# Optimization experiments

Measured on AMD Instinct MI355X. Metric: run time of the kernel, lower is better.

The kernel has to match this reference:

```python
import jax, jax.numpy as jnp
import numpy as np

DIM = 192
HEADS = 8
EPS = 1e-12  # torch F.normalize eps


def setup_inputs() -> dict:
    key = jax.random.key(0)
    k1, k2, k3, k4 = jax.random.split(key, 4)
    b, c, h, w = 2, DIM, 256, 256
    x = jax.random.normal(k1, (b, c, h, w), dtype=jnp.float32)
    # 1x1 conv weights stored as (out, in)
    qkv_w = jax.random.normal(k2, (3 * c, c), dtype=jnp.float32) * (1.0 / np.sqrt(c))
    # depthwise 3x3, groups = 3c -> OIHW with I=1
    dw_w = jax.random.normal(k3, (3 * c, 1, 3, 3), dtype=jnp.float32) * (1.0 / 3.0)
    proj_w = jax.random.normal(k4, (c, c), dtype=jnp.float32) * (1.0 / np.sqrt(c))
    temperature = jnp.ones((HEADS, 1, 1), dtype=jnp.float32)
    return {"x": x, "qkv_w": qkv_w, "dw_w": dw_w, "proj_w": proj_w,
            "temperature": temperature}


def _l2norm(t):
    n = jnp.sqrt(jnp.sum(t * t, axis=-1, keepdims=True))
    return t / jnp.maximum(n, EPS)


def reference(x, qkv_w, dw_w, proj_w, temperature):
    b, c, h, w = x.shape
    # 1x1 conv (pointwise) -> depthwise 3x3 conv
    qkv = jnp.einsum('oc,bchw->bohw', qkv_w, x)  # (b, 3c, h, w)
    qkv = jax.lax.conv_general_dilated(
        qkv, dw_w, window_strides=(1, 1), padding='SAME',
        feature_group_count=3 * c,
        dimension_numbers=('NCHW', 'OIHW', 'NCHW'))
    q, k, v = jnp.split(qkv, 3, axis=1)
    # faithful reshape: full C channels per head, spatial dim split by heads
    q = q.reshape(b, HEADS, c, -1)
    k = k.reshape(b, HEADS, c, -1)
    v = v.reshape(b, HEADS, c, -1)
    q = _l2norm(q)
    k = _l2norm(k)
    attn = jnp.einsum('bhcn,bhdn->bhcd', q, k) * temperature  # (b,H,c,c)
    attn = jax.nn.softmax(attn, axis=-1)
    out = jnp.einsum('bhcd,bhdn->bhcn', attn, v)
    out = out.reshape(b, c, h, w)
    out = jnp.einsum('oc,bchw->bohw', proj_w, out)
    return out
```

## Files before the change

### kernel.cpp

```cpp
#include <hip/hip_runtime.h>
#include <math.h>

typedef unsigned short u16;
typedef unsigned int   u32;
typedef short bf16x8 __attribute__((ext_vector_type(8)));
typedef float f32x4  __attribute__((ext_vector_type(4)));
typedef u16 u16x8 __attribute__((ext_vector_type(8)));
typedef u32 u32x4 __attribute__((ext_vector_type(4)));

#define MFMA16(a,b,c) __builtin_amdgcn_mfma_f32_16x16x32_bf16((a),(b),(c),0,0,0)

__device__ __forceinline__ float bf2f(u16 h){ u32 u=((u32)h)<<16; return __uint_as_float(u); }
__device__ __forceinline__ u16 f2bf(float f){ u32 u=__float_as_uint(f); return (u16)((u+0x7fffu+((u>>16)&1u))>>16); }
__device__ __forceinline__ u32 pack2(float a, float b){ return (u32)f2bf(a) | ((u32)f2bf(b)<<16); }

__device__ __forceinline__ void gl2lds(const u16* g, u16* l){
  __builtin_amdgcn_global_load_lds((const __attribute__((address_space(1))) u32*)g,
                                   (__attribute__((address_space(3))) u32*)l, 16, 0, 0);
}
__device__ __forceinline__ void stc(u16* p, float v){ *p = f2bf(v); }
__device__ __forceinline__ void stc(float* p, float v){ *p = v; }
__device__ __forceinline__ void ld4(const u16* p, float* v){ ushort4 x=*(const ushort4*)p; v[0]=bf2f(x.x);v[1]=bf2f(x.y);v[2]=bf2f(x.z);v[3]=bf2f(x.w); }

__device__ __forceinline__ int xcd_remap(){
  int gx = gridDim.x, gy = gridDim.y;
  int lin = blockIdx.x + gx*(blockIdx.y + gy*blockIdx.z);
  int nwg = gx*gy*gridDim.z;
  if (nwg & 7) return lin;
  int q = nwg >> 3;
  return (lin & 7)*q + (lin >> 3);
}

__global__ void prep_kernel(const float* __restrict__ qkv_w, const float* __restrict__ proj_w,
                            u16* __restrict__ wq, u16* __restrict__ wp, float* __restrict__ norms){
  int i = blockIdx.x*256 + threadIdx.x;
  if (i < 110592) wq[i] = f2bf(qkv_w[i]);
  else if (i < 147456) wp[i-110592] = f2bf(proj_w[i-110592]);
  else if (i < 156672) norms[i-147456] = 0.f;
}

__global__ __launch_bounds__(256) void transpose_kernel(
    const u16* __restrict__ in, u16* __restrict__ out,
    long in_hi, long in_lo, long out_slab, int in_pitch)
{
  __shared__ float tile[64][65];
  const int t = threadIdx.x;
  const int z = blockIdx.z;
  const u16* ip = in + (long)(z>>3)*in_hi + (long)(z&7)*in_lo;
  u16* op = out + (long)z*out_slab;
  const int s0 = blockIdx.x*64, c0 = blockIdx.y*64;
  const int rl = t>>4, cc = (t&15)*4;
#pragma unroll
  for (int rr=0; rr<4; rr++){
    int row = rr*16 + rl;
    float v[4];
    ld4(ip + (long)(c0+row)*in_pitch + s0 + cc, v);
    tile[row][cc+0]=v[0]; tile[row][cc+1]=v[1]; tile[row][cc+2]=v[2]; tile[row][cc+3]=v[3];
  }
  __syncthreads();
#pragma unroll
  for (int wr=0; wr<4; wr++){
    int sl = wr*16 + rl;
    ushort4 s;
    s.x = f2bf(tile[cc+0][sl]); s.y = f2bf(tile[cc+1][sl]);
    s.z = f2bf(tile[cc+2][sl]); s.w = f2bf(tile[cc+3][sl]);
    *(ushort4*)(op + (long)(s0+sl)*192 + c0 + cc) = s;
  }
}

__global__ __launch_bounds__(256) void gemm_qkv_kernel(
    const u16* __restrict__ A, const float* __restrict__ X, u16* __restrict__ C)
{
  __shared__ __align__(16) u16 As[128*32];
  __shared__ __align__(16) u16 Bs[128*36];
  const int t = threadIdx.x, w = t>>6, l = t&63;
  const int wrk = xcd_remap();
  const int mt = wrk % 5;
  const int rest = wrk / 5;
  const int nt = rest % 512, bz = rest / 512;
  const int m0 = mt*128, n0 = nt*128;
  const float* Xb = X + (long)bz*12582912L + n0;
  const int rq = t>>2, qq = (t&3)*8;
  int ar0 = m0 + rq;      if (ar0 >= 576) ar0 = 575;
  int ar1 = m0 + 64 + rq; if (ar1 >= 576) ar1 = 575;
  const int bq = t&31;
  const int kb = (t>>5)*4;
  f32x4 acc[4][4];
#pragma unroll
  for (int i=0;i<4;i++)
#pragma unroll
    for (int j=0;j<4;j++) acc[i][j] = f32x4{0.f,0.f,0.f,0.f};

  for (int k0=0; k0<192; k0+=32){
    __syncthreads();
    float xv[4][4];
#pragma unroll
    for (int i=0;i<4;i++){
      const float* xr = Xb + (long)(k0+kb+i)*65536 + bq;
#pragma unroll
      for (int c=0;c<4;c++) xv[i][c] = xr[c*32];
    }
    gl2lds(A + (long)ar0*192 + k0 + qq, As + t*8);
    gl2lds(A + (long)ar1*192 + k0 + qq, As + (256+t)*8);
#pragma unroll
    for (int c=0;c<4;c++){
      u16* bw = Bs + (bq + c*32)*36 + kb;
      *(u32*)(bw)     = pack2(xv[0][c], xv[1][c]);
      *(u32*)(bw + 2) = pack2(xv[2][c], xv[3][c]);
    }
    __syncthreads();
    const u16* ap = As + ((w>>1)*64 + (l&15))*32 + (l>>4)*8;
    const u16* bp = Bs + ((w&1)*64 + (l&15))*36 + (l>>4)*8;
    bf16x8 a[4], b[4];
#pragma unroll
    for (int i=0;i<4;i++) a[i] = *(const bf16x8*)(ap + i*512);
#pragma unroll
    for (int j=0;j<4;j++){
      uint2 p0 = *(const uint2*)(bp + j*576);
      uint2 p1 = *(const uint2*)(bp + j*576 + 4);
      u32x4 tv = {p0.x, p0.y, p1.x, p1.y};
      b[j] = __builtin_bit_cast(bf16x8, tv);
    }
#pragma unroll
    for (int i=0;i<4;i++)
#pragma unroll
      for (int j=0;j<4;j++) acc[i][j] = MFMA16(a[i], b[j], acc[i][j]);
  }
  const int mw = m0 + (w>>1)*64, nw = n0 + (w&1)*64;
  u16* Cb = C + (long)bz*37748736L;
#pragma unroll
  for (int i=0;i<4;i++){
#pragma unroll
    for (int r=0;r<4;r++){
      int row = mw + i*16 + (l>>4)*4 + r;
      if (row < 576){
        u16* cp = Cb + (long)row*65536 + nw + (l&15);
#pragma unroll
        for (int j=0;j<4;j++) stc(cp + j*16, acc[i][j][r]);
      }
    }
  }
}

template<typename TC>
__global__ __launch_bounds__(256) void gemm_nt_kernel(
    const u16* __restrict__ A, const u16* __restrict__ B, TC* __restrict__ C,
    int M, long sB, long sC)
{
  __shared__ __align__(16) u16 As[128*32];
  __shared__ __align__(16) u16 Bs[128*32];
  const int t = threadIdx.x, w = t>>6, l = t&63;
  const int wrk = xcd_remap();
  const int mt = wrk % gridDim.x;
  const int rest = wrk / gridDim.x;
  const int nt = rest % gridDim.y, bz = rest / gridDim.y;
  const int m0 = mt*128, n0 = nt*128;
  const u16* Bb = B + (long)bz*sB + (long)n0*192;
  const int rq = t>>2, qq = (t&3)*8;
  int ar0 = m0 + rq;      if (ar0 >= M) ar0 = M-1;
  int ar1 = m0 + 64 + rq; if (ar1 >= M) ar1 = M-1;
  f32x4 acc[4][4];
#pragma unroll
  for (int i=0;i<4;i++)
#pragma unroll
    for (int j=0;j<4;j++) acc[i][j] = f32x4{0.f,0.f,0.f,0.f};

  for (int k0=0; k0<192; k0+=32){
    __syncthreads();
    gl2lds(A + (long)ar0*192 + k0 + qq, As + t*8);
    gl2lds(A + (long)ar1*192 + k0 + qq, As + (256+t)*8);
    gl2lds(Bb + (long)rq*192 + k0 + qq, Bs + t*8);
    gl2lds(Bb + (long)(64+rq)*192 + k0 + qq, Bs + (256+t)*8);
    __syncthreads();
    const u16* ap = As + ((w>>1)*64 + (l&15))*32 + (l>>4)*8;
    const u16* bp = Bs + ((w&1)*64 + (l&15))*32 + (l>>4)*8;
    bf16x8 a[4], b[4];
#pragma unroll
    for (int i=0;i<4;i++){ a[i] = *(const bf16x8*)(ap + i*512); b[i] = *(const bf16x8*)(bp + i*512); }
#pragma unroll
    for (int i=0;i<4;i++)
#pragma unroll
      for (int j=0;j<4;j++) acc[i][j] = MFMA16(a[i], b[j], acc[i][j]);
  }
  const int mw = m0 + (w>>1)*64, nw = n0 + (w&1)*64;
  TC* Cb = C + (long)bz*sC;
#pragma unroll
  for (int i=0;i<4;i++){
#pragma unroll
    for (int r=0;r<4;r++){
      int row = mw + i*16 + (l>>4)*4 + r;
      if (row < M){
        TC* cp = Cb + (long)row*65536 + nw + (l&15);
#pragma unroll
        for (int j=0;j<4;j++) stc(cp + j*16, acc[i][j][r]);
      }
    }
  }
}

__global__ __launch_bounds__(256) void dwconv_kernel(
    const u16* __restrict__ in, const float* __restrict__ w9s,
    u16* __restrict__ out, float* __restrict__ norms)
{
  const int bo = blockIdx.x >> 1;
  const int half = blockIdx.x & 1;
  const int o  = bo % 576;
  const int t = threadIdx.x, wv = t>>6, l = t&63;
  const int q = l&31;
  const int r0 = half*128 + wv*32 + (l>>5)*16;
  const u16* ip = in + (long)bo*65536L + q*8;
  u16* op = out + (long)bo*65536L + q*8;
  float w[9];
#pragma unroll
  for (int i=0;i<9;i++) w[i] = w9s[o*9+i];
  float ap[8], ac[8], an[8];
#pragma unroll
  for (int c=0;c<8;c++){ ap[c]=0.f; ac[c]=0.f; }
  float ss = 0.f;
#pragma unroll
  for (int it=0; it<18; ++it){
    const int g = r0 - 1 + it;
    float v[8];
    if (g>=0 && g<256){
      u16x8 u = *(const u16x8*)(ip + g*256);
#pragma unroll
      for (int c=0;c<8;c++) v[c] = bf2f(u[c]);
    } else {
#pragma unroll
      for (int c=0;c<8;c++) v[c]=0.f;
    }
    float slv = __shfl(v[7], (l+63)&63);
    float srv = __shfl(v[0], (l+1)&63);
    const float lf  = (q==0)  ? 0.f : slv;
    const float rgt = (q==31) ? 0.f : srv;
#pragma unroll
    for (int c=0;c<8;c++){
      const float le = (c==0) ? lf  : v[c-1];
      const float mi = v[c];
      const float ri = (c==7) ? rgt : v[c+1];
      ap[c] = fmaf(w[6],le, fmaf(w[7],mi, fmaf(w[8],ri, ap[c])));
      ac[c] = fmaf(w[3],le, fmaf(w[4],mi, fmaf(w[5],ri, ac[c])));
      an[c] = fmaf(w[0],le, fmaf(w[1],mi, w[2]*ri));
    }
    if (it >= 2){
      u16x8 s;
#pragma unroll
      for (int c=0;c<8;c++){ s[c] = f2bf(ap[c]); ss = fmaf(ap[c],ap[c],ss); }
      *(u16x8*)(op + (g-1)*256) = s;
    }
#pragma unroll
    for (int c=0;c<8;c++){ ap[c]=ac[c]; ac[c]=an[c]; }
  }
#pragma unroll
  for (int off=32; off>=1; off>>=1) ss += __shfl_xor(ss, off);
  if (o < 384 && l == 0)
    norms[bo*8 + half*4 + wv] = ss;
}

__global__ __launch_bounds__(256) void gemm_qk_kernel(
    const u16* __restrict__ conv, float* __restrict__ part)
{
  __shared__ __align__(16) u16 As[64*64];
  __shared__ __align__(16) u16 Bs[64*64];
  const int t = threadIdx.x, w = t>>6, l = t&63;
  const int wrk = xcd_remap();
  const int mt = wrk % 3;
  const int rest = wrk / 3;
  const int nt = rest % 3, z = rest / 3;
  const int bh = z>>3, sl = z&7;
  const int b = bh>>3, h = bh&7;
  const u16* Q  = conv + (long)b*37748736L + (long)h*1572864L;
  const u16* Kp = Q + 12582912L;
  const int m0 = mt*64, n0 = nt*64;
  const int rq = t>>3, qq = (t&7)*8;
  const long qo0 = (long)(m0+rq)*8192 + qq;
  const long qo1 = (long)(m0+32+rq)*8192 + qq;
  const long ko0 = (long)(n0+rq)*8192 + qq;
  const long ko1 = (long)(n0+32+rq)*8192 + qq;
  f32x4 acc[2][2];
#pragma unroll
  for (int i=0;i<2;i++)
#pragma unroll
    for (int j=0;j<2;j++) acc[i][j] = f32x4{0.f,0.f,0.f,0.f};
  const int kbeg = sl*1024;
  for (int k0=kbeg; k0<kbeg+1024; k0+=64){
    __syncthreads();
    gl2lds(Q  + qo0 + k0, As + t*8);
    gl2lds(Q  + qo1 + k0, As + (256+t)*8);
    gl2lds(Kp + ko0 + k0, Bs + t*8);
    gl2lds(Kp + ko1 + k0, Bs + (256+t)*8);
    __syncthreads();
    const u16* ap = As + ((w>>1)*32 + (l&15))*64 + (l>>4)*8;
    const u16* bp = Bs + ((w&1)*32 + (l&15))*64 + (l>>4)*8;
#pragma unroll
    for (int ks=0; ks<2; ks++){
      bf16x8 a0 = *(const bf16x8*)(ap + ks*32);
      bf16x8 a1 = *(const bf16x8*)(ap + 1024 + ks*32);
      bf16x8 b0 = *(const bf16x8*)(bp + ks*32);
      bf16x8 b1 = *(const bf16x8*)(bp + 1024 + ks*32);
      acc[0][0]=MFMA16(a0,b0,acc[0][0]); acc[0][1]=MFMA16(a0,b1,acc[0][1]);
      acc[1][0]=MFMA16(a1,b0,acc[1][0]); acc[1][1]=MFMA16(a1,b1,acc[1][1]);
    }
  }
  float* P = part + (long)z*36864L;
  const int mw = m0 + (w>>1)*32, nw = n0 + (w&1)*32;
#pragma unroll
  for (int i=0;i<2;i++)
#pragma unroll
    for (int j=0;j<2;j++)
#pragma unroll
      for (int r=0;r<4;r++)
        P[(long)(mw + i*16 + (l>>4)*4 + r)*192 + nw + j*16 + (l&15)] = acc[i][j][r];
}

__global__ __launch_bounds__(256) void softmax_kernel(
    const float* __restrict__ part, const float* __restrict__ temp,
    const float* __restrict__ norms, u16* __restrict__ attn)
{
  const int t = threadIdx.x, wv = t>>6, l = t&63;
  const int rg = blockIdx.x*4 + wv;
  const int bh = rg/192, r = rg - bh*192;
  const int b = bh>>3, h = bh&7;
  const float tp = temp[h];
  const float sq = norms[(b*576 + 24*h + (r>>3))*8 + (r&7)];
  const float invq = 1.f/fmaxf(sqrtf(sq), 1e-12f);
  const float* P = part + (long)bh*8L*36864L + (long)r*192;
  float lv[3];
#pragma unroll
  for (int j=0;j<3;j++){
    int col = l + j*64;
    float s = 0.f;
#pragma unroll
    for (int ks=0; ks<8; ks++) s += P[(long)ks*36864L + col];
    float sk = norms[(b*576 + 192 + 24*h + (col>>3))*8 + (col&7)];
    float invk = 1.f/fmaxf(sqrtf(sk), 1e-12f);
    lv[j] = s*invq*invk*tp;
  }
  float mx = fmaxf(lv[0], fmaxf(lv[1], lv[2]));
#pragma unroll
  for (int o=32;o>=1;o>>=1) mx = fmaxf(mx, __shfl_xor(mx, o));
  float e[3], sum = 0.f;
#pragma unroll
  for (int j=0;j<3;j++){ e[j] = expf(lv[j]-mx); sum += e[j]; }
#pragma unroll
  for (int o=32;o>=1;o>>=1) sum += __shfl_xor(sum, o);
  const float inv = 1.f/sum;
  u16* ap = attn + (long)bh*36864L + (long)r*192;
#pragma unroll
  for (int j=0;j<3;j++) ap[l + j*64] = f2bf(e[j]*inv);
}

__global__ __launch_bounds__(256) void gemm_av_kernel(
    const u16* __restrict__ VT, const u16* __restrict__ attn, u16* __restrict__ out_sc)
{
  __shared__ __align__(16) char smem[69632];
  u16* As = (u16*)smem;
  u16* Bs = (u16*)(smem + 8192);
  const int t = threadIdx.x, w = t>>6, l = t&63;
  const int wrk = xcd_remap();
  const int mt = wrk % 64;
  const int rest = wrk / 64;
  const int nt = rest % 2, bh = rest / 2;
  const int b = bh>>3, h = bh&7;
  const u16* Av = VT + (long)bh*1572864L;
  const u16* Bt = attn + (long)bh*36864L;
  const int m0 = mt*128, n0 = nt*128;
  const int rq = t>>2, qq = (t&3)*8;
  int br0 = n0 + rq;      if (br0 > 191) br0 = 191;
  int br1 = n0 + 64 + rq; if (br1 > 191) br1 = 191;
  f32x4 acc[4][4];
#pragma unroll
  for (int i=0;i<4;i++)
#pragma unroll
    for (int j=0;j<4;j++) acc[i][j] = f32x4{0.f,0.f,0.f,0.f};
  for (int k0=0; k0<192; k0+=32){
    __syncthreads();
    gl2lds(Av + (long)(m0+rq)*192 + k0 + qq, As + t*8);
    gl2lds(Av + (long)(m0+64+rq)*192 + k0 + qq, As + (256+t)*8);
    gl2lds(Bt + (long)br0*192 + k0 + qq, Bs + t*8);
    gl2lds(Bt + (long)br1*192 + k0 + qq, Bs + (256+t)*8);
    __syncthreads();
    const u16* ap = As + ((w>>1)*64 + (l&15))*32 + (l>>4)*8;
    const u16* bp = Bs + ((w&1)*64 + (l&15))*32 + (l>>4)*8;
    bf16x8 a[4], bb[4];
#pragma unroll
    for (int i=0;i<4;i++){ a[i] = *(const bf16x8*)(ap + i*512); bb[i] = *(const bf16x8*)(bp + i*512); }
#pragma unroll
    for (int i=0;i<4;i++)
#pragma unroll
      for (int j=0;j<4;j++) acc[i][j] = MFMA16(a[i], bb[j], acc[i][j]);
  }
  __syncthreads();
  float* wb = (float*)smem + w*4352;
#pragma unroll
  for (int i=0;i<4;i++)
#pragma unroll
    for (int j=0;j<4;j++)
#pragma unroll
      for (int r=0;r<4;r++)
        wb[(i*16 + (l>>4)*4 + r)*68 + j*16 + (l&15)] = acc[i][j][r];
  __syncthreads();
  const int c0w = nt*128 + (w&1)*64;
  if (c0w < 192){
    const int cb = 24*h + (c0w>>3);
    const int mw = m0 + (w>>1)*64;
    u16* ob = out_sc + (long)b*12582912L + cb;
    const int nl0 = l>>3, sb = l&7;
#pragma unroll
    for (int ri=0; ri<8; ri++){
      int nl = ri*8 + nl0;
      const float* src = wb + nl*68 + sb;
      u32 d0 = (u32)f2bf(src[0])  | ((u32)f2bf(src[8])  << 16);
      u32 d1 = (u32)f2bf(src[16]) | ((u32)f2bf(src[24]) << 16);
      u32 d2 = (u32)f2bf(src[32]) | ((u32)f2bf(src[40]) << 16);
      u32 d3 = (u32)f2bf(src[48]) | ((u32)f2bf(src[56]) << 16);
      *(uint4*)(ob + ((long)sb*8192 + mw + nl)*192) = make_uint4(d0,d1,d2,d3);
    }
  }
}

extern "C" void kernel_launch(void* const* d_in, const int* in_sizes, int n_in,
                              void* d_out, int out_size, void* d_ws, size_t ws_size,
                              hipStream_t stream)
{
  const float* x      = (const float*)d_in[0];
  const float* qkv_w  = (const float*)d_in[1];
  const float* dw_w   = (const float*)d_in[2];
  const float* proj_w = (const float*)d_in[3];
  const float* temp   = (const float*)d_in[4];
  float* out = (float*)d_out;

  char* ws = (char*)d_ws;
  u16*   conv    = (u16*)(ws + 0);
  u16*   qkv_raw = (u16*)(ws + 150994944);
  u16*   VT      = (u16*)(ws + 150994944);
  u16*   out_sc  = (u16*)(ws + 201326592);
  float* part    = (float*)(ws + 251658240);
  u16*   attn    = (u16*)(ws + 270532608);
  u16*   wq_bf   = (u16*)(ws + 301989888);
  u16*   wp_bf   = (u16*)(ws + 302211072);
  float* norms   = (float*)(ws + 302284800);

  prep_kernel<<<dim3(612), 256, 0, stream>>>(qkv_w, proj_w, wq_bf, wp_bf, norms);

  gemm_qkv_kernel<<<dim3(5, 512, 2), 256, 0, stream>>>(wq_bf, x, qkv_raw);

  dwconv_kernel<<<dim3(1152*2), 256, 0, stream>>>(qkv_raw, dw_w, conv, norms);

  transpose_kernel<<<dim3(128, 3, 16), 256, 0, stream>>>(
      conv + 25165824L, VT, 37748736L, 1572864L, 1572864L, 8192);

  gemm_qk_kernel<<<dim3(3, 3, 128), 256, 0, stream>>>(conv, part);

  softmax_kernel<<<dim3(768), 256, 0, stream>>>(part, temp, norms, attn);

  gemm_av_kernel<<<dim3(64, 2, 16), 256, 0, stream>>>(VT, attn, out_sc);

  gemm_nt_kernel<float><<<dim3(2, 512, 2), 256, 0, stream>>>(
      wp_bf, out_sc, out, 192, 12582912L, 12582912L);
}
```

Before: 464.6 us.

## Double-buffer LDS tiles in QKV GEMM to overlap loads with MFMA

Splits the A and B shared-memory tiles of the QKV projection GEMM into two buffers. The next K-slice is prefetched into the alternate buffer (global X loads into registers, A via direct global-to-LDS loads) while MFMAs run on the current one, so only one barrier per iteration remains. This is meant to hide global memory latency behind compute, at the cost of doubled LDS use, which may reduce occupancy, and more live registers for the prefetched values.

```diff
diff --git a/kernel.cpp b/kernel.cpp
--- a/kernel.cpp
+++ b/kernel.cpp
@@ -71,8 +71,8 @@
 __global__ __launch_bounds__(256) void gemm_qkv_kernel(
     const u16* __restrict__ A, const float* __restrict__ X, u16* __restrict__ C)
 {
-  __shared__ __align__(16) u16 As[128*32];
-  __shared__ __align__(16) u16 Bs[128*36];
+  __shared__ __align__(16) u16 As[2][128*32];
+  __shared__ __align__(16) u16 Bs[2][128*36];
   const int t = threadIdx.x, w = t>>6, l = t&63;
   const int wrk = xcd_remap();
   const int mt = wrk % 5;
@@ -91,26 +91,42 @@
 #pragma unroll
     for (int j=0;j<4;j++) acc[i][j] = f32x4{0.f,0.f,0.f,0.f};
 
-  for (int k0=0; k0<192; k0+=32){
-    __syncthreads();
+  {
     float xv[4][4];
 #pragma unroll
     for (int i=0;i<4;i++){
-      const float* xr = Xb + (long)(k0+kb+i)*65536 + bq;
+      const float* xr = Xb + (long)(kb+i)*65536 + bq;
 #pragma unroll
       for (int c=0;c<4;c++) xv[i][c] = xr[c*32];
     }
-    gl2lds(A + (long)ar0*192 + k0 + qq, As + t*8);
-    gl2lds(A + (long)ar1*192 + k0 + qq, As + (256+t)*8);
+    gl2lds(A + (long)ar0*192 + qq, As[0] + t*8);
+    gl2lds(A + (long)ar1*192 + qq, As[0] + (256+t)*8);
 #pragma unroll
     for (int c=0;c<4;c++){
-      u16* bw = Bs + (bq + c*32)*36 + kb;
+      u16* bw = Bs[0] + (bq + c*32)*36 + kb;
       *(u32*)(bw)     = pack2(xv[0][c], xv[1][c]);
       *(u32*)(bw + 2) = pack2(xv[2][c], xv[3][c]);
     }
-    __syncthreads();
-    const u16* ap = As + ((w>>1)*64 + (l&15))*32 + (l>>4)*8;
-    const u16* bp = Bs + ((w&1)*64 + (l&15))*36 + (l>>4)*8;
+  }
+  __syncthreads();
+
+  int cur = 0;
+#pragma unroll
+  for (int k0=0; k0<192; k0+=32){
+    const int nxt = cur^1;
+    float nv[4][4];
+    if (k0 < 160){
+#pragma unroll
+      for (int i=0;i<4;i++){
+        const float* xr = Xb + (long)(k0+32+kb+i)*65536 + bq;
+#pragma unroll
+        for (int c=0;c<4;c++) nv[i][c] = xr[c*32];
+      }
+      gl2lds(A + (long)ar0*192 + k0+32 + qq, As[nxt] + t*8);
+      gl2lds(A + (long)ar1*192 + k0+32 + qq, As[nxt] + (256+t)*8);
+    }
+    const u16* ap = As[cur] + ((w>>1)*64 + (l&15))*32 + (l>>4)*8;
+    const u16* bp = Bs[cur] + ((w&1)*64 + (l&15))*36 + (l>>4)*8;
     bf16x8 a[4], b[4];
 #pragma unroll
     for (int i=0;i<4;i++) a[i] = *(const bf16x8*)(ap + i*512);
@@ -125,6 +141,16 @@
     for (int i=0;i<4;i++)
 #pragma unroll
       for (int j=0;j<4;j++) acc[i][j] = MFMA16(a[i], b[j], acc[i][j]);
+    if (k0 < 160){
+#pragma unroll
+      for (int c=0;c<4;c++){
+        u16* bw = Bs[nxt] + (bq + c*32)*36 + kb;
+        *(u32*)(bw)     = pack2(nv[0][c], nv[1][c]);
+        *(u32*)(bw + 2) = pack2(nv[2][c], nv[3][c]);
+      }
+      __syncthreads();
+      cur = nxt;
+    }
   }
   const int mw = m0 + (w>>1)*64, nw = n0 + (w&1)*64;
   u16* Cb = C + (long)bz*37748736L;
```

Result: no change. 468.2 us (+0.8%).
